# Kernel tuning notes

Hardware: AMD Instinct MI355X
Metric: run time of the kernel (lower is better)

Reference implementation:

```python
import jax, jax.numpy as jnp
import numpy as np

H, I, E, TOPK = 2048, 4096, 8, 2
B, S = 2, 2048

def setup_inputs() -> dict:
    key = jax.random.key(0)
    ks = jax.random.split(key, 6)
    x = jax.random.normal(ks[0], (B, S, H), dtype=jnp.float32)
    expert_indices = jax.random.randint(ks[1], (B, S, TOPK), 0, E, dtype=jnp.int64)
    expert_weights = jax.random.uniform(ks[2], (B, S, TOPK), dtype=jnp.float32)
    gate_proj = jax.random.normal(ks[3], (E, I, H), dtype=jnp.float32) * 0.02
    up_proj = jax.random.normal(ks[4], (E, I, H), dtype=jnp.float32) * 0.02
    down_proj = jax.random.normal(ks[5], (E, H, I), dtype=jnp.float32) * 0.02
    return {"x": x, "expert_indices": expert_indices, "expert_weights": expert_weights,
            "gate_proj": gate_proj, "up_proj": up_proj, "down_proj": down_proj}

def reference(x, expert_indices, expert_weights, gate_proj, up_proj, down_proj):
    b, s, h = x.shape
    T = b * s
    xf = x.reshape(T, h)                                   # [T, H]
    idx = expert_indices.reshape(T, -1)                    # [T, K]
    w = expert_weights.reshape(T, -1)                      # [T, K]
    n_exp = gate_proj.shape[0]
    # Per-token combined weight for each expert (sums duplicate slots, matching
    # the original weighted scatter-add over (token, slot) pairs).
    onehot = jax.nn.one_hot(idx, n_exp, dtype=xf.dtype)    # [T, K, E]
    we = jnp.einsum('tk,tke->et', w, onehot)               # [E, T]

    def step(acc, inp):
        g_w, u_w, d_w, w_e = inp                           # [I,H], [I,H], [H,I], [T]
        g = xf @ g_w.T                                     # [T, I]
        u = xf @ u_w.T                                     # [T, I]
        inter = g * jax.nn.sigmoid(g) * u                  # fused SiLU(g) * u
        acc = acc + w_e[:, None] * (inter @ d_w.T)         # weighted combine
        return acc, None

    out0 = jnp.zeros((T, h), dtype=x.dtype)
    out, _ = jax.lax.scan(step, out0, (gate_proj, up_proj, down_proj, we))
    return out.reshape(b, s, h)
```

## Files before the change

kernel.cpp:

```cpp
#include <hip/hip_runtime.h>
#include <hip/hip_bf16.h>
#include <stdint.h>

#define H_DIM 2048
#define I_DIM 4096
#define NEXP  8
#define NTOK  4096
#define NPAIR 8192
#define PAD_ROWS (NPAIR + 128)

#define WS_COUNTS   0ull
#define WS_OFFSETS  256ull
#define WS_TOKID    1024ull
#define WS_PAIRW    (64ull * 1024)
#define WS_XG       (1ull * 1024 * 1024)
#define WS_INTER    (40ull * 1024 * 1024)
#define WS_NEEDED   (WS_INTER + (unsigned long long)PAD_ROWS * I_DIM * 2)

typedef __attribute__((ext_vector_type(8))) short bf16x8;
typedef __attribute__((ext_vector_type(4))) float f32x4;

#if defined(__has_builtin)
#if __has_builtin(__builtin_amdgcn_cvt_pk_bf16_f32)
#define HAVE_CVT_PK 1
#endif
#endif

__device__ __forceinline__ uint32_t bf16_bits_rne(float x) {
  uint32_t u = __float_as_uint(x);
  return (u + 0x7FFFu + ((u >> 16) & 1u)) >> 16;
}

__device__ __forceinline__ uint32_t pk_bf16(float a, float b) {
#ifdef HAVE_CVT_PK
  auto r = __builtin_amdgcn_cvt_pk_bf16_f32(a, b);
  return __builtin_bit_cast(uint32_t, r);
#else
  return bf16_bits_rne(a) | (bf16_bits_rne(b) << 16);
#endif
}

__device__ __forceinline__ uint16_t bf16_one(float x) {
  return (uint16_t)(pk_bf16(x, x) & 0xFFFFu);
}

__device__ __forceinline__ void async_load16(const void* g, void* l) {
  __builtin_amdgcn_global_load_lds(
      (const __attribute__((address_space(1))) void*)g,
      (__attribute__((address_space(3))) void*)l, 16, 0, 0);
}

__global__ void route_kernel(const int* __restrict__ idx, const float* __restrict__ wts,
                             int* __restrict__ ws_counts, int* __restrict__ ws_offsets,
                             int* __restrict__ tokid, float* __restrict__ pairw) {
  __shared__ int s_cnt[NEXP], s_off[NEXP], s_cur[NEXP];
  int tid = threadIdx.x;
  if (tid < NEXP) s_cnt[tid] = 0;
  __syncthreads();
  for (int p = tid; p < NPAIR; p += 256) atomicAdd(&s_cnt[idx[p]], 1);
  __syncthreads();
  if (tid == 0) {
    int acc = 0;
    for (int e = 0; e < NEXP; e++) { s_off[e] = acc; s_cur[e] = acc; acc += s_cnt[e]; }
  }
  __syncthreads();
  for (int p = tid; p < NPAIR; p += 256) {
    int e = idx[p];
    int slot = atomicAdd(&s_cur[e], 1);
    tokid[slot] = p >> 1;
    pairw[slot] = wts[p];
  }
  if (tid < NEXP) { ws_counts[tid] = s_cnt[tid]; ws_offsets[tid] = s_off[tid]; }
}

__global__ void gather_cast_kernel(const float* __restrict__ x, const int* __restrict__ tokid,
                                   uint16_t* __restrict__ xg) {
  int p = blockIdx.x;
  int t = tokid[p];
  int c = threadIdx.x * 8;
  const float4* src = (const float4*)(x + (size_t)t * H_DIM + c);
  float4 v0 = src[0], v1 = src[1];
  uint4 o;
  o.x = pk_bf16(v0.x, v0.y); o.y = pk_bf16(v0.z, v0.w);
  o.z = pk_bf16(v1.x, v1.y); o.w = pk_bf16(v1.z, v1.w);
  *(uint4*)(xg + (size_t)p * H_DIM + c) = o;
}

__global__ __launch_bounds__(256, 2)
void gemm1_kernel(const uint16_t* __restrict__ xg,
                  const float* __restrict__ gate, const float* __restrict__ up,
                  const int* __restrict__ ws_counts, const int* __restrict__ ws_offsets,
                  uint16_t* __restrict__ inter) {
  int e = blockIdx.z;
  int cnt = ws_counts[e];
  int rowTile = blockIdx.y;
  if (rowTile * 128 >= cnt) return;
  int off = ws_offsets[e];
  int colBase = blockIdx.x * 128;
  size_t rowBase = (size_t)off + (size_t)rowTile * 128;

  __shared__ uint16_t lA[128 * 64];
  __shared__ uint16_t lBg[128 * 64];
  __shared__ uint16_t lBu[128 * 64];

  int tid = threadIdx.x;
  int lane = tid & 63, wid = tid >> 6;
  int wm = (wid & 1) * 64, wn = (wid >> 1) * 64;
  int lcol = lane & 15, quad = lane >> 4;

  const float* gbase = gate + (size_t)e * I_DIM * H_DIM + (size_t)colBase * H_DIM;
  const float* ubase = up   + (size_t)e * I_DIM * H_DIM + (size_t)colBase * H_DIM;

  f32x4 accg[4][4], accu[4][4];
  f32x4 zero = {0.f, 0.f, 0.f, 0.f};
#pragma unroll
  for (int mi = 0; mi < 4; mi++)
#pragma unroll
    for (int ni = 0; ni < 4; ni++) { accg[mi][ni] = zero; accu[mi][ni] = zero; }

  for (int k0 = 0; k0 < H_DIM; k0 += 64) {
    __syncthreads();
#pragma unroll
    for (int rd = 0; rd < 4; rd++) {
      int chunkBase = rd * 256 + wid * 64;
      int chunk = chunkBase + lane;
      int row = chunk >> 3, kc = (chunk & 7) * 8;
      async_load16(xg + (rowBase + row) * H_DIM + k0 + kc, lA + chunkBase * 8);
    }
#pragma unroll
    for (int it = 0; it < 4; it++) {
      int c = it * 256 + tid;
      int row = c >> 3, kc = (c & 7) * 8;
      size_t soff = (size_t)row * H_DIM + k0 + kc;
      const float4* sg = (const float4*)(gbase + soff);
      float4 g0 = sg[0], g1 = sg[1];
      const float4* su = (const float4*)(ubase + soff);
      float4 u0 = su[0], u1 = su[1];
      uint4 og = { pk_bf16(g0.x, g0.y), pk_bf16(g0.z, g0.w), pk_bf16(g1.x, g1.y), pk_bf16(g1.z, g1.w) };
      uint4 ou = { pk_bf16(u0.x, u0.y), pk_bf16(u0.z, u0.w), pk_bf16(u1.x, u1.y), pk_bf16(u1.z, u1.w) };
      *(uint4*)(lBg + c * 8) = og;
      *(uint4*)(lBu + c * 8) = ou;
    }
    __syncthreads();
#pragma unroll
    for (int ks = 0; ks < 64; ks += 32) {
      int krow = ks + quad * 8;
      bf16x8 af[4], bg[4], bu[4];
#pragma unroll
      for (int mi = 0; mi < 4; mi++)
        af[mi] = *(const bf16x8*)(lA + (wm + mi * 16 + lcol) * 64 + krow);
#pragma unroll
      for (int ni = 0; ni < 4; ni++) {
        bg[ni] = *(const bf16x8*)(lBg + (wn + ni * 16 + lcol) * 64 + krow);
        bu[ni] = *(const bf16x8*)(lBu + (wn + ni * 16 + lcol) * 64 + krow);
      }
#pragma unroll
      for (int mi = 0; mi < 4; mi++)
#pragma unroll
        for (int ni = 0; ni < 4; ni++) {
          accg[mi][ni] = __builtin_amdgcn_mfma_f32_16x16x32_bf16(af[mi], bg[ni], accg[mi][ni], 0, 0, 0);
          accu[mi][ni] = __builtin_amdgcn_mfma_f32_16x16x32_bf16(af[mi], bu[ni], accu[mi][ni], 0, 0, 0);
        }
    }
  }
  int col0 = colBase + wn;
#pragma unroll
  for (int mi = 0; mi < 4; mi++) {
#pragma unroll
    for (int r = 0; r < 4; r++) {
      int localRow = rowTile * 128 + wm + mi * 16 + quad * 4 + r;
      if (localRow < cnt) {
        size_t prow = (size_t)off + localRow;
#pragma unroll
        for (int ni = 0; ni < 4; ni++) {
          float g = accg[mi][ni][r], u = accu[mi][ni][r];
          float v = (g / (1.f + __expf(-g))) * u;
          inter[prow * I_DIM + col0 + ni * 16 + lcol] = bf16_one(v);
        }
      }
    }
  }
}

__global__ __launch_bounds__(256, 2)
void gemm2_kernel(const uint16_t* __restrict__ inter, const float* __restrict__ down,
                  const int* __restrict__ ws_counts, const int* __restrict__ ws_offsets,
                  const int* __restrict__ tokid, const float* __restrict__ pairw,
                  float* __restrict__ out) {
  int e = blockIdx.z;
  int cnt = ws_counts[e];
  int rowTile = blockIdx.y;
  if (rowTile * 128 >= cnt) return;
  int off = ws_offsets[e];
  int colBase = blockIdx.x * 128;
  size_t rowBase = (size_t)off + (size_t)rowTile * 128;

  __shared__ uint16_t lA[128 * 64];
  __shared__ uint16_t lB[128 * 64];

  int tid = threadIdx.x;
  int lane = tid & 63, wid = tid >> 6;
  int wm = (wid & 1) * 64, wn = (wid >> 1) * 64;
  int lcol = lane & 15, quad = lane >> 4;

  const float* dbase = down + (size_t)e * H_DIM * I_DIM + (size_t)colBase * I_DIM;

  f32x4 acc[4][4];
  f32x4 zero = {0.f, 0.f, 0.f, 0.f};
#pragma unroll
  for (int mi = 0; mi < 4; mi++)
#pragma unroll
    for (int ni = 0; ni < 4; ni++) acc[mi][ni] = zero;

  for (int k0 = 0; k0 < I_DIM; k0 += 64) {
    __syncthreads();
#pragma unroll
    for (int rd = 0; rd < 4; rd++) {
      int chunkBase = rd * 256 + wid * 64;
      int chunk = chunkBase + lane;
      int row = chunk >> 3, kc = (chunk & 7) * 8;
      async_load16(inter + (rowBase + row) * I_DIM + k0 + kc, lA + chunkBase * 8);
    }
#pragma unroll
    for (int it = 0; it < 4; it++) {
      int c = it * 256 + tid;
      int row = c >> 3, kc = (c & 7) * 8;
      const float4* sd = (const float4*)(dbase + (size_t)row * I_DIM + k0 + kc);
      float4 d0 = sd[0], d1 = sd[1];
      uint4 od = { pk_bf16(d0.x, d0.y), pk_bf16(d0.z, d0.w), pk_bf16(d1.x, d1.y), pk_bf16(d1.z, d1.w) };
      *(uint4*)(lB + c * 8) = od;
    }
    __syncthreads();
#pragma unroll
    for (int ks = 0; ks < 64; ks += 32) {
      int krow = ks + quad * 8;
      bf16x8 af[4], bf[4];
#pragma unroll
      for (int mi = 0; mi < 4; mi++)
        af[mi] = *(const bf16x8*)(lA + (wm + mi * 16 + lcol) * 64 + krow);
#pragma unroll
      for (int ni = 0; ni < 4; ni++)
        bf[ni] = *(const bf16x8*)(lB + (wn + ni * 16 + lcol) * 64 + krow);
#pragma unroll
      for (int mi = 0; mi < 4; mi++)
#pragma unroll
        for (int ni = 0; ni < 4; ni++)
          acc[mi][ni] = __builtin_amdgcn_mfma_f32_16x16x32_bf16(af[mi], bf[ni], acc[mi][ni], 0, 0, 0);
    }
  }
  int col0 = colBase + wn;
#pragma unroll
  for (int mi = 0; mi < 4; mi++) {
#pragma unroll
    for (int r = 0; r < 4; r++) {
      int localRow = rowTile * 128 + wm + mi * 16 + quad * 4 + r;
      if (localRow < cnt) {
        size_t prow = (size_t)off + localRow;
        int t = tokid[prow];
        float w = pairw[prow];
        float* orow = out + (size_t)t * H_DIM + col0;
#pragma unroll
        for (int ni = 0; ni < 4; ni++)
          atomicAdd(orow + ni * 16 + lcol, acc[mi][ni][r] * w);
      }
    }
  }
}

extern "C" void kernel_launch(void* const* d_in, const int* in_sizes, int n_in,
                              void* d_out, int out_size, void* d_ws, size_t ws_size,
                              hipStream_t stream) {
  const float* x    = (const float*)d_in[0];
  const int*   eidx = (const int*)d_in[1];
  const float* ew   = (const float*)d_in[2];
  const float* gate = (const float*)d_in[3];
  const float* up   = (const float*)d_in[4];
  const float* down = (const float*)d_in[5];
  float* out = (float*)d_out;
  char* ws = (char*)d_ws;

  if (ws_size < WS_NEEDED) {
    hipMemsetAsync(d_out, 0, (size_t)NTOK * H_DIM * sizeof(float), stream);
    return;
  }

  int*      counts  = (int*)(ws + WS_COUNTS);
  int*      offsets = (int*)(ws + WS_OFFSETS);
  int*      tokid   = (int*)(ws + WS_TOKID);
  float*    pairw   = (float*)(ws + WS_PAIRW);
  uint16_t* xg      = (uint16_t*)(ws + WS_XG);
  uint16_t* inter   = (uint16_t*)(ws + WS_INTER);

  hipMemsetAsync(d_out, 0, (size_t)NTOK * H_DIM * sizeof(float), stream);
  route_kernel<<<1, 256, 0, stream>>>(eidx, ew, counts, offsets, tokid, pairw);
  gather_cast_kernel<<<NPAIR, 256, 0, stream>>>(x, tokid, xg);
  gemm1_kernel<<<dim3(I_DIM / 128, NPAIR / 128, NEXP), 256, 0, stream>>>(
      xg, gate, up, counts, offsets, inter);
  gemm2_kernel<<<dim3(H_DIM / 128, NPAIR / 128, NEXP), 256, 0, stream>>>(
      inter, down, counts, offsets, tokid, pairw, out);
}
```

Baseline: 1.415 ms.

## Pre-cast expert weights to bf16 and replace atomic scatter with slot buffer combine

When the workspace is large enough, a new kernel casts the gate, up and down weights to bf16 in workspace on every call. New GEMM kernels then stream both operands straight into LDS with async global-to-LDS loads, instead of reading fp32 weights inside the GEMM. The second GEMM writes weighted per-slot rows to a dense buffer, and a combine kernel sums each token's two slots. This removes the output memset and the atomicAdd scatter. In exchange it adds about 1.2 GB of cast traffic per call and needs about 560 MiB of workspace; with less workspace the old path still runs.

```diff
diff --git a/kernel.cpp b/kernel.cpp
--- a/kernel.cpp
+++ b/kernel.cpp
@@ -9,13 +9,20 @@
 #define NPAIR 8192
 #define PAD_ROWS (NPAIR + 128)
 
+#define MiB (1024ull * 1024ull)
 #define WS_COUNTS   0ull
 #define WS_OFFSETS  256ull
 #define WS_TOKID    1024ull
-#define WS_PAIRW    (64ull * 1024)
-#define WS_XG       (1ull * 1024 * 1024)
-#define WS_INTER    (40ull * 1024 * 1024)
-#define WS_NEEDED   (WS_INTER + (unsigned long long)PAD_ROWS * I_DIM * 2)
+#define WS_SLOT     (64ull * 1024)
+#define WS_PAIRW    (128ull * 1024)
+#define WS_XG       (1ull * MiB)
+#define WS_INTER    (36ull * MiB)
+#define WS_Y        (104ull * MiB)
+#define WS_GW       (176ull * MiB)
+#define WS_UW       (304ull * MiB)
+#define WS_DW       (432ull * MiB)
+#define WS_FULL     (560ull * MiB)
+#define WS_MIN_NEEDED (WS_INTER + (unsigned long long)PAD_ROWS * I_DIM * 2)
 
 typedef __attribute__((ext_vector_type(8))) short bf16x8;
 typedef __attribute__((ext_vector_type(4))) float f32x4;
@@ -52,7 +59,8 @@
 
 __global__ void route_kernel(const int* __restrict__ idx, const float* __restrict__ wts,
                              int* __restrict__ ws_counts, int* __restrict__ ws_offsets,
-                             int* __restrict__ tokid, float* __restrict__ pairw) {
+                             int* __restrict__ tokid, int* __restrict__ slotOf,
+                             float* __restrict__ pairw) {
   __shared__ int s_cnt[NEXP], s_off[NEXP], s_cur[NEXP];
   int tid = threadIdx.x;
   if (tid < NEXP) s_cnt[tid] = 0;
@@ -68,6 +76,7 @@
     int e = idx[p];
     int slot = atomicAdd(&s_cur[e], 1);
     tokid[slot] = p >> 1;
+    slotOf[p] = slot;
     pairw[slot] = wts[p];
   }
   if (tid < NEXP) { ws_counts[tid] = s_cnt[tid]; ws_offsets[tid] = s_off[tid]; }
@@ -84,6 +93,196 @@
   o.x = pk_bf16(v0.x, v0.y); o.y = pk_bf16(v0.z, v0.w);
   o.z = pk_bf16(v1.x, v1.y); o.w = pk_bf16(v1.z, v1.w);
   *(uint4*)(xg + (size_t)p * H_DIM + c) = o;
+}
+
+__global__ void cast3_kernel(const float* __restrict__ g, const float* __restrict__ u,
+                             const float* __restrict__ d,
+                             uint16_t* __restrict__ gw, uint16_t* __restrict__ uw,
+                             uint16_t* __restrict__ dw) {
+  const float* src = blockIdx.y == 0 ? g : (blockIdx.y == 1 ? u : d);
+  uint16_t*    dst = blockIdx.y == 0 ? gw : (blockIdx.y == 1 ? uw : dw);
+  const long long n8 = (long long)NEXP * I_DIM * H_DIM / 8;
+  long long stride = (long long)gridDim.x * blockDim.x;
+  for (long long i = (long long)blockIdx.x * blockDim.x + threadIdx.x; i < n8; i += stride) {
+    const float4* s = (const float4*)(src + i * 8);
+    float4 a = s[0], b = s[1];
+    uint4 o = { pk_bf16(a.x, a.y), pk_bf16(a.z, a.w), pk_bf16(b.x, b.y), pk_bf16(b.z, b.w) };
+    *(uint4*)(dst + i * 8) = o;
+  }
+}
+
+__global__ __launch_bounds__(256, 2)
+void gemm1_pre_kernel(const uint16_t* __restrict__ xg,
+                      const uint16_t* __restrict__ gw, const uint16_t* __restrict__ uw,
+                      const int* __restrict__ ws_counts, const int* __restrict__ ws_offsets,
+                      uint16_t* __restrict__ inter) {
+  int e = blockIdx.z;
+  int cnt = ws_counts[e];
+  int rowTile = blockIdx.y;
+  if (rowTile * 128 >= cnt) return;
+  int off = ws_offsets[e];
+  int colBase = blockIdx.x * 128;
+  size_t rowBase = (size_t)off + (size_t)rowTile * 128;
+
+  __shared__ uint16_t lA[128 * 64];
+  __shared__ uint16_t lBg[128 * 64];
+  __shared__ uint16_t lBu[128 * 64];
+
+  int tid = threadIdx.x;
+  int lane = tid & 63, wid = tid >> 6;
+  int wm = (wid & 1) * 64, wn = (wid >> 1) * 64;
+  int lcol = lane & 15, quad = lane >> 4;
+
+  const uint16_t* gwb = gw + ((size_t)e * I_DIM + colBase) * H_DIM;
+  const uint16_t* uwb = uw + ((size_t)e * I_DIM + colBase) * H_DIM;
+
+  f32x4 accg[4][4], accu[4][4];
+  f32x4 zero = {0.f, 0.f, 0.f, 0.f};
+#pragma unroll
+  for (int mi = 0; mi < 4; mi++)
+#pragma unroll
+    for (int ni = 0; ni < 4; ni++) { accg[mi][ni] = zero; accu[mi][ni] = zero; }
+
+  for (int k0 = 0; k0 < H_DIM; k0 += 64) {
+    __syncthreads();
+#pragma unroll
+    for (int rd = 0; rd < 4; rd++) {
+      int chunkBase = rd * 256 + wid * 64;
+      int chunk = chunkBase + lane;
+      int row = chunk >> 3, kc = (chunk & 7) * 8;
+      size_t goff = (size_t)row * H_DIM + k0 + kc;
+      async_load16(xg + (rowBase + row) * H_DIM + k0 + kc, lA + chunkBase * 8);
+      async_load16(gwb + goff, lBg + chunkBase * 8);
+      async_load16(uwb + goff, lBu + chunkBase * 8);
+    }
+    __syncthreads();
+#pragma unroll
+    for (int ks = 0; ks < 64; ks += 32) {
+      int krow = ks + quad * 8;
+      bf16x8 af[4], bg[4], bu[4];
+#pragma unroll
+      for (int mi = 0; mi < 4; mi++)
+        af[mi] = *(const bf16x8*)(lA + (wm + mi * 16 + lcol) * 64 + krow);
+#pragma unroll
+      for (int ni = 0; ni < 4; ni++) {
+        bg[ni] = *(const bf16x8*)(lBg + (wn + ni * 16 + lcol) * 64 + krow);
+        bu[ni] = *(const bf16x8*)(lBu + (wn + ni * 16 + lcol) * 64 + krow);
+      }
+#pragma unroll
+      for (int mi = 0; mi < 4; mi++)
+#pragma unroll
+        for (int ni = 0; ni < 4; ni++) {
+          accg[mi][ni] = __builtin_amdgcn_mfma_f32_16x16x32_bf16(af[mi], bg[ni], accg[mi][ni], 0, 0, 0);
+          accu[mi][ni] = __builtin_amdgcn_mfma_f32_16x16x32_bf16(af[mi], bu[ni], accu[mi][ni], 0, 0, 0);
+        }
+    }
+  }
+  int col0 = colBase + wn;
+#pragma unroll
+  for (int mi = 0; mi < 4; mi++) {
+#pragma unroll
+    for (int r = 0; r < 4; r++) {
+      int localRow = rowTile * 128 + wm + mi * 16 + quad * 4 + r;
+      if (localRow < cnt) {
+        size_t prow = (size_t)off + localRow;
+#pragma unroll
+        for (int ni = 0; ni < 4; ni++) {
+          float g = accg[mi][ni][r], u = accu[mi][ni][r];
+          float v = (g / (1.f + __expf(-g))) * u;
+          inter[prow * I_DIM + col0 + ni * 16 + lcol] = bf16_one(v);
+        }
+      }
+    }
+  }
+}
+
+__global__ __launch_bounds__(256, 2)
+void gemm2_pre_kernel(const uint16_t* __restrict__ inter, const uint16_t* __restrict__ dw,
+                      const int* __restrict__ ws_counts, const int* __restrict__ ws_offsets,
+                      const float* __restrict__ pairw, float* __restrict__ y) {
+  int e = blockIdx.z;
+  int cnt = ws_counts[e];
+  int rowTile = blockIdx.y;
+  if (rowTile * 128 >= cnt) return;
+  int off = ws_offsets[e];
+  int colBase = blockIdx.x * 128;
+  size_t rowBase = (size_t)off + (size_t)rowTile * 128;
+
+  __shared__ uint16_t lA[128 * 64];
+  __shared__ uint16_t lB[128 * 64];
+
+  int tid = threadIdx.x;
+  int lane = tid & 63, wid = tid >> 6;
+  int wm = (wid & 1) * 64, wn = (wid >> 1) * 64;
+  int lcol = lane & 15, quad = lane >> 4;
+
+  const uint16_t* dwb = dw + ((size_t)e * H_DIM + colBase) * I_DIM;
+
+  f32x4 acc[4][4];
+  f32x4 zero = {0.f, 0.f, 0.f, 0.f};
+#pragma unroll
+  for (int mi = 0; mi < 4; mi++)
+#pragma unroll
+    for (int ni = 0; ni < 4; ni++) acc[mi][ni] = zero;
+
+  for (int k0 = 0; k0 < I_DIM; k0 += 64) {
+    __syncthreads();
+#pragma unroll
+    for (int rd = 0; rd < 4; rd++) {
+      int chunkBase = rd * 256 + wid * 64;
+      int chunk = chunkBase + lane;
+      int row = chunk >> 3, kc = (chunk & 7) * 8;
+      async_load16(inter + (rowBase + row) * I_DIM + k0 + kc, lA + chunkBase * 8);
+      async_load16(dwb + (size_t)row * I_DIM + k0 + kc, lB + chunkBase * 8);
+    }
+    __syncthreads();
+#pragma unroll
+    for (int ks = 0; ks < 64; ks += 32) {
+      int krow = ks + quad * 8;
+      bf16x8 af[4], bf[4];
+#pragma unroll
+      for (int mi = 0; mi < 4; mi++)
+        af[mi] = *(const bf16x8*)(lA + (wm + mi * 16 + lcol) * 64 + krow);
+#pragma unroll
+      for (int ni = 0; ni < 4; ni++)
+        bf[ni] = *(const bf16x8*)(lB + (wn + ni * 16 + lcol) * 64 + krow);
+#pragma unroll
+      for (int mi = 0; mi < 4; mi++)
+#pragma unroll
+        for (int ni = 0; ni < 4; ni++)
+          acc[mi][ni] = __builtin_amdgcn_mfma_f32_16x16x32_bf16(af[mi], bf[ni], acc[mi][ni], 0, 0, 0);
+    }
+  }
+  int col0 = colBase + wn;
+#pragma unroll
+  for (int mi = 0; mi < 4; mi++) {
+#pragma unroll
+    for (int r = 0; r < 4; r++) {
+      int localRow = rowTile * 128 + wm + mi * 16 + quad * 4 + r;
+      if (localRow < cnt) {
+        size_t prow = (size_t)off + localRow;
+        float w = pairw[prow];
+        float* yr = y + prow * H_DIM + col0;
+#pragma unroll
+        for (int ni = 0; ni < 4; ni++)
+          yr[ni * 16 + lcol] = acc[mi][ni][r] * w;
+      }
+    }
+  }
+}
+
+__global__ void combine_kernel(const float* __restrict__ y, const int* __restrict__ slotOf,
+                               float* __restrict__ out) {
+  int t = blockIdx.x;
+  int s0 = slotOf[2 * t], s1 = slotOf[2 * t + 1];
+  int c = threadIdx.x * 8;
+  const float4* a = (const float4*)(y + (size_t)s0 * H_DIM + c);
+  const float4* b = (const float4*)(y + (size_t)s1 * H_DIM + c);
+  float4 a0 = a[0], a1 = a[1], b0 = b[0], b1 = b[1];
+  float4 o0 = {a0.x + b0.x, a0.y + b0.y, a0.z + b0.z, a0.w + b0.w};
+  float4 o1 = {a1.x + b1.x, a1.y + b1.y, a1.z + b1.z, a1.w + b1.w};
+  float4* dst = (float4*)(out + (size_t)t * H_DIM + c);
+  dst[0] = o0; dst[1] = o1;
 }
 
 __global__ __launch_bounds__(256, 2)
@@ -279,7 +478,7 @@
   float* out = (float*)d_out;
   char* ws = (char*)d_ws;
 
-  if (ws_size < WS_NEEDED) {
+  if (ws_size < WS_MIN_NEEDED) {
     hipMemsetAsync(d_out, 0, (size_t)NTOK * H_DIM * sizeof(float), stream);
     return;
   }
@@ -287,15 +486,31 @@
   int*      counts  = (int*)(ws + WS_COUNTS);
   int*      offsets = (int*)(ws + WS_OFFSETS);
   int*      tokid   = (int*)(ws + WS_TOKID);
+  int*      slotOf  = (int*)(ws + WS_SLOT);
   float*    pairw   = (float*)(ws + WS_PAIRW);
   uint16_t* xg      = (uint16_t*)(ws + WS_XG);
   uint16_t* inter   = (uint16_t*)(ws + WS_INTER);
 
-  hipMemsetAsync(d_out, 0, (size_t)NTOK * H_DIM * sizeof(float), stream);
-  route_kernel<<<1, 256, 0, stream>>>(eidx, ew, counts, offsets, tokid, pairw);
+  route_kernel<<<1, 256, 0, stream>>>(eidx, ew, counts, offsets, tokid, slotOf, pairw);
   gather_cast_kernel<<<NPAIR, 256, 0, stream>>>(x, tokid, xg);
-  gemm1_kernel<<<dim3(I_DIM / 128, NPAIR / 128, NEXP), 256, 0, stream>>>(
-      xg, gate, up, counts, offsets, inter);
-  gemm2_kernel<<<dim3(H_DIM / 128, NPAIR / 128, NEXP), 256, 0, stream>>>(
-      inter, down, counts, offsets, tokid, pairw, out);
-}
+
+  if (ws_size >= WS_FULL) {
+    float*    y  = (float*)(ws + WS_Y);
+    uint16_t* gw = (uint16_t*)(ws + WS_GW);
+    uint16_t* uw = (uint16_t*)(ws + WS_UW);
+    uint16_t* dwp = (uint16_t*)(ws + WS_DW);
+
+    cast3_kernel<<<dim3(1024, 3), 256, 0, stream>>>(gate, up, down, gw, uw, dwp);
+    gemm1_pre_kernel<<<dim3(I_DIM / 128, NPAIR / 128, NEXP), 256, 0, stream>>>(
+        xg, gw, uw, counts, offsets, inter);
+    gemm2_pre_kernel<<<dim3(H_DIM / 128, NPAIR / 128, NEXP), 256, 0, stream>>>(
+        inter, dwp, counts, offsets, pairw, (float*)(ws + WS_Y));
+    combine_kernel<<<NTOK, 256, 0, stream>>>(y, slotOf, out);
+  } else {
+    hipMemsetAsync(d_out, 0, (size_t)NTOK * H_DIM * sizeof(float), stream);
+    gemm1_kernel<<<dim3(I_DIM / 128, NPAIR / 128, NEXP), 256, 0, stream>>>(
+        xg, gate, up, counts, offsets, inter);
+    gemm2_kernel<<<dim3(H_DIM / 128, NPAIR / 128, NEXP), 256, 0, stream>>>(
+        inter, down, counts, offsets, tokid, pairw, out);
+  }
+}
```

Measured after the change: 1.434 ms. Within noise of the previous version (+1.3%).
